# Kernel optimization log

Hardware: AMD Instinct MI355X
Metric: run time of the kernel (lower is better)

The kernel has to match this reference:

```python
import jax, jax.numpy as jnp
import numpy as np

TOKENS, IN_F, OUT_F, R = 8192, 4096, 4096, 16
NS_STEPS = 5
NS_EPS = 1e-7


def newtonschulz5(G, steps=NS_STEPS, eps=NS_EPS):
    # Quintic Newton-Schulz orthogonalization: sigma -> 1, preserving U, V.
    a, b, c = 3.4445, -4.775, 2.0315
    X = G / (jnp.linalg.norm(G) + eps)
    transposed = G.shape[0] > G.shape[1]
    if transposed:
        X = X.T
    for _ in range(steps):
        A = X @ X.T                 # [m, m]
        B = b * A + c * (A @ A)
        X = a * X + B @ X
    if transposed:
        X = X.T
    return X


def setup_inputs() -> dict:
    key = jax.random.key(0)
    kx, kw, kb, ka, kbb = jax.random.split(key, 5)
    x = jax.random.normal(kx, (TOKENS, IN_F), dtype=jnp.float32)
    # base linear params
    W = jax.random.normal(kw, (OUT_F, IN_F), dtype=jnp.float32) / np.sqrt(IN_F)
    bias = jax.random.normal(kb, (OUT_F,), dtype=jnp.float32) * 0.01
    # LoRA params: A ~ orthogonal-ish rows, B small (init_scale/sqrt(out*r))
    lora_A = jax.random.normal(ka, (R, IN_F), dtype=jnp.float32) / np.sqrt(IN_F)
    init_std = 0.01 / np.sqrt(OUT_F * R)
    lora_B = jax.random.normal(kbb, (OUT_F, R), dtype=jnp.float32) * init_std
    return {"x": x, "W": W, "bias": bias, "lora_A": lora_A, "lora_B": lora_B}


def reference(x, W, bias, lora_A, lora_B):
    # base_out = x @ W^T + bias
    base_out = x @ W.T + bias
    # G = B A  (full [out, in] materialization, as in the original)
    G = lora_B @ lora_A
    alpha = jnp.linalg.norm(G)
    M = newtonschulz5(G)
    # lora_dropout = 0 -> identity
    lora_out = x @ M.T
    return base_out + alpha * lora_out
```

## Files before the change

### kernel.cpp

```cpp
#include <hip/hip_runtime.h>
#include <hip/hip_bf16.h>
#include <math.h>

#define TOKENS 8192
#define IN_F   4096
#define OUT_F  4096
#define LR     16

typedef __bf16 bf16_t;
typedef __attribute__((ext_vector_type(8)))  __bf16 bf16x8;
typedef __attribute__((ext_vector_type(4)))  __bf16 bf16x4;
typedef __attribute__((ext_vector_type(4)))  float  floatx4;
typedef __attribute__((ext_vector_type(16))) float  floatx16;

#define GL2LDS(gp, lp) \
    __builtin_amdgcn_global_load_lds((const __attribute__((address_space(1))) unsigned int*)(gp), \
                                     (__attribute__((address_space(3))) unsigned int*)(lp), 16, 0, 0)

__global__ void pq_kernel(const float* __restrict__ A, const float* __restrict__ B,
                          float* __restrict__ P, float* __restrict__ Q) {
    __shared__ float red[256];
    const int b = blockIdx.x, t = threadIdx.x;
    float s = 0.f;
    if (b < 256) {
        const int i = b >> 4, j = b & 15;
        const float* ai = A + (size_t)i * IN_F;
        const float* aj = A + (size_t)j * IN_F;
        for (int k = t; k < IN_F; k += 256) s += ai[k] * aj[k];
    } else {
        const int i = (b - 256) >> 4, j = (b - 256) & 15;
        for (int k = t; k < OUT_F; k += 256) s += B[k * LR + i] * B[k * LR + j];
    }
    red[t] = s; __syncthreads();
    for (int off = 128; off > 0; off >>= 1) {
        if (t < off) red[t] += red[t + off];
        __syncthreads();
    }
    if (t == 0) {
        if (b < 256) P[b] = red[0];
        else         Q[b - 256] = red[0];
    }
}

__global__ void ns_kernel(const float* __restrict__ P, const float* __restrict__ Q,
                          float* __restrict__ Sc) {
    __shared__ double Ps[256], Qs[256], Ss[256], Ys[256], Zs[256], Ts[256], Us[256], Vs[256];
    __shared__ double alpha_s, inv_n;
    const int t = threadIdx.x, i = t >> 4, j = t & 15;
    Ps[t] = P[t]; Qs[t] = Q[t];
    __syncthreads();
    if (t == 0) {
        double s = 0.0;
        for (int a = 0; a < 16; ++a)
            for (int b2 = 0; b2 < 16; ++b2) s += Ps[a * 16 + b2] * Qs[b2 * 16 + a];
        const double al = sqrt(s);
        alpha_s = al;
        inv_n   = 1.0 / (al + 1e-7);
    }
    __syncthreads();
    Ss[t] = (i == j) ? inv_n : 0.0;
    __syncthreads();
    const double ca = 3.4445, cb = -4.775, cc = 2.0315;
    for (int step = 0; step < 5; ++step) {
        double s;
        s = 0; for (int q = 0; q < 16; ++q) s += Ss[i*16+q] * Ps[q*16+j]; Ys[t] = s; __syncthreads();
        s = 0; for (int q = 0; q < 16; ++q) s += Ys[i*16+q] * Ss[j*16+q]; Zs[t] = s; __syncthreads();
        s = 0; for (int q = 0; q < 16; ++q) s += Zs[i*16+q] * Qs[q*16+j]; Ts[t] = s; __syncthreads();
        s = 0; for (int q = 0; q < 16; ++q) s += Ts[i*16+q] * Ss[q*16+j]; Us[t] = s; __syncthreads();
        s = 0; for (int q = 0; q < 16; ++q) s += Ts[i*16+q] * Us[q*16+j]; Vs[t] = s; __syncthreads();
        Ss[t] = ca * Ss[t] + cb * Us[t] + cc * Vs[t];
        __syncthreads();
    }
    Sc[t] = (float)(alpha_s * Ss[t]);
}

__global__ void sca_kernel(const float* __restrict__ Sc, const float* __restrict__ A,
                           float* __restrict__ ScA) {
    const int idx = blockIdx.x * 256 + threadIdx.x;
    const int r = idx >> 12, i = idx & 4095;
    float s = 0.f;
    for (int q = 0; q < 16; ++q) s += Sc[r * 16 + q] * A[q * IN_F + i];
    ScA[r * IN_F + i] = s;
}

__global__ void prep_kernel(const float* __restrict__ x, bf16_t* __restrict__ Xb,
                            const float* __restrict__ W, const float* __restrict__ Bm,
                            const float* __restrict__ ScA, bf16_t* __restrict__ Wb) {
    const int b = blockIdx.x, t = threadIdx.x;
    if (b < 32768) {
        const int idx = b * 256 + t;
        const float4 u = ((const float4*)x)[idx];
        bf16x4 v;
        v[0] = (__bf16)u.x; v[1] = (__bf16)u.y; v[2] = (__bf16)u.z; v[3] = (__bf16)u.w;
        ((bf16x4*)Xb)[idx] = v;
        return;
    }
    const int bb = b - 32768;
    const int o0 = (bb >> 2) * 4;
    const int i  = (bb & 3) * 1024 + t * 4;
    float4 acc[4];
    #pragma unroll
    for (int r = 0; r < 4; ++r) acc[r] = *(const float4*)&W[(size_t)(o0 + r) * IN_F + i];
    #pragma unroll
    for (int q = 0; q < LR; ++q) {
        const float4 sa = *(const float4*)&ScA[q * IN_F + i];
        #pragma unroll
        for (int r = 0; r < 4; ++r) {
            const float bq = Bm[(o0 + r) * LR + q];
            acc[r].x += bq * sa.x; acc[r].y += bq * sa.y;
            acc[r].z += bq * sa.z; acc[r].w += bq * sa.w;
        }
    }
    #pragma unroll
    for (int r = 0; r < 4; ++r) {
        bf16x4 v;
        v[0] = (__bf16)acc[r].x; v[1] = (__bf16)acc[r].y;
        v[2] = (__bf16)acc[r].z; v[3] = (__bf16)acc[r].w;
        *(bf16x4*)&Wb[(size_t)(o0 + r) * IN_F + i] = v;
    }
}

#define GBM 256
#define GBN 256
#define GBK 32
#define GNT (IN_F / GBK)

__global__ __launch_bounds__(512, 2) void gemm_kernel(
        const bf16_t* __restrict__ Xb, const bf16_t* __restrict__ Wb,
        const float* __restrict__ bias, float* __restrict__ out) {
    __shared__ bf16_t lds[3 * 16384];
    const int t = threadIdx.x;
    const int lane = t & 63, wv = t >> 6;
    const int wm = wv & 1, wn = wv >> 1;
    const int ln = lane & 31, kg = lane >> 5;

    const int bid = blockIdx.x;
    const int swz = (bid & 7) * 64 + (bid >> 3);
    const int mt = swz & 31, nt = swz >> 5;
    const int m0 = mt * GBM, n0 = nt * GBN;

    const int g_lrow = t >> 3, g_sp = t & 7;
    const int g_sl = g_sp ^ (g_lrow & 7);
    const int g_r  = (g_lrow << 1) | (g_sl >> 2);
    const int g_k0 = (g_sl & 3) * 8;
    const bf16_t* srcA0 = Xb + (size_t)(m0 + g_r) * IN_F + g_k0;
    const bf16_t* srcA1 = srcA0 + (size_t)128 * IN_F;
    const bf16_t* srcB0 = Wb + (size_t)(n0 + g_r) * IN_F + g_k0;
    const bf16_t* srcB1 = srcB0 + (size_t)128 * IN_F;
    const int dA0 = t * 8, dA1 = 4096 + t * 8;

#define STAGE(buf, kt) do { \
        GL2LDS(srcA0 + (size_t)(kt) * GBK, (buf) + dA0); \
        GL2LDS(srcA1 + (size_t)(kt) * GBK, (buf) + dA1); \
        GL2LDS(srcB0 + (size_t)(kt) * GBK, (buf) + 8192 + dA0); \
        GL2LDS(srcB1 + (size_t)(kt) * GBK, (buf) + 8192 + dA1); \
    } while (0)

    const int rx  = (ln >> 1) & 7;
    const int sl0 = ((((ln & 1) << 2) | kg)       ^ rx) * 8;
    const int sl1 = ((((ln & 1) << 2) | (2 + kg)) ^ rx) * 8;
    const int aRow = (wm * 64 + (ln >> 1)) * 64;
    const int bRow = 8192 + (wn * 32 + (ln >> 1)) * 64;

    floatx16 acc[4][2];
    #pragma unroll
    for (int mf = 0; mf < 4; ++mf)
        #pragma unroll
        for (int nf = 0; nf < 2; ++nf)
            acc[mf][nf] = (floatx16)(0.0f);

    bf16_t* bc = &lds[0];
    bf16_t* bn = &lds[16384];
    bf16_t* bs = &lds[32768];

    STAGE(bc, 0);
    STAGE(bn, 1);
    asm volatile("s_waitcnt vmcnt(4)" ::: "memory");
    __builtin_amdgcn_s_barrier();
    asm volatile("" ::: "memory");

    for (int kt = 0; kt < GNT; ++kt) {
        if (kt + 2 < GNT) STAGE(bs, kt + 2);

        bf16x8 a0[4], a1[4], b0[2], b1[2];
        #pragma unroll
        for (int mf = 0; mf < 4; ++mf) {
            a0[mf] = *(const bf16x8*)&bc[aRow + mf * 1024 + sl0];
            a1[mf] = *(const bf16x8*)&bc[aRow + mf * 1024 + sl1];
        }
        #pragma unroll
        for (int nf = 0; nf < 2; ++nf) {
            b0[nf] = *(const bf16x8*)&bc[bRow + nf * 1024 + sl0];
            b1[nf] = *(const bf16x8*)&bc[bRow + nf * 1024 + sl1];
        }

        __builtin_amdgcn_s_barrier();
        asm volatile("" ::: "memory");
        __builtin_amdgcn_s_setprio(1);
        #pragma unroll
        for (int mf = 0; mf < 4; ++mf)
            #pragma unroll
            for (int nf = 0; nf < 2; ++nf)
                acc[mf][nf] = __builtin_amdgcn_mfma_f32_32x32x16_bf16(a0[mf], b0[nf], acc[mf][nf], 0, 0, 0);
        #pragma unroll
        for (int mf = 0; mf < 4; ++mf)
            #pragma unroll
            for (int nf = 0; nf < 2; ++nf)
                acc[mf][nf] = __builtin_amdgcn_mfma_f32_32x32x16_bf16(a1[mf], b1[nf], acc[mf][nf], 0, 0, 0);
        __builtin_amdgcn_s_setprio(0);

        if (kt < GNT - 2) asm volatile("s_waitcnt vmcnt(4)" ::: "memory");
        else              asm volatile("s_waitcnt vmcnt(0)" ::: "memory");
        __builtin_amdgcn_s_barrier();
        asm volatile("" ::: "memory");

        bf16_t* tmp = bc; bc = bn; bn = bs; bs = tmp;
    }
#undef STAGE

    const int colb = n0 + wn * 64 + ln;
    const int rowb = m0 + wm * 128 + 4 * kg;
    const float bv0 = bias[colb];
    const float bv1 = bias[colb + 32];
    #pragma unroll
    for (int mf = 0; mf < 4; ++mf) {
        #pragma unroll
        for (int rg = 0; rg < 16; ++rg) {
            const int row = rowb + mf * 32 + (rg & 3) + 8 * (rg >> 2);
            out[(size_t)row * OUT_F + colb]      = acc[mf][0][rg] + bv0;
            out[(size_t)row * OUT_F + colb + 32] = acc[mf][1][rg] + bv1;
        }
    }
}

extern "C" void kernel_launch(void* const* d_in, const int* in_sizes, int n_in,
                              void* d_out, int out_size, void* d_ws, size_t ws_size,
                              hipStream_t stream) {
    const float* x    = (const float*)d_in[0];
    const float* W    = (const float*)d_in[1];
    const float* bias = (const float*)d_in[2];
    const float* lA_  = (const float*)d_in[3];
    const float* lB_  = (const float*)d_in[4];
    float* out = (float*)d_out;

    char* ws = (char*)d_ws;
    bf16_t* Xb  = (bf16_t*)ws;
    bf16_t* Wb  = (bf16_t*)(ws + 67108864);
    float*  ScA = (float*)(ws + 100663296);
    float*  P   = (float*)(ws + 100925440);
    float*  Q   = P + 256;
    float*  Sc  = Q + 256;

    pq_kernel  <<<512, 256, 0, stream>>>(lA_, lB_, P, Q);
    ns_kernel  <<<1, 256, 0, stream>>>(P, Q, Sc);
    sca_kernel <<<256, 256, 0, stream>>>(Sc, lA_, ScA);
    prep_kernel<<<36864, 256, 0, stream>>>(x, Xb, W, lB_, ScA, Wb);
    gemm_kernel<<<512, 512, 0, stream>>>(Xb, Wb, bias, out);
}
```

Measured before the change: 578.4 us.

## Restructure GEMM main loop into 8-phase pipeline with 16x16x32 MFMA and BK=64

Rewrites the bf16 GEMM main loop. Each K tile of 64 is split into two 32-wide halves, and each half is split into M-half phases. LDS fragment loads, global-to-LDS staging of the next tile and MFMA bursts are interleaved, with barriers between phases. The MFMA shape moves from 32x32x16 to 16x16x32 (8x4 fragments per wave), and LDS is double-buffered over 128 KB. The intent is to overlap memory traffic with matrix math more finely and cut per-iteration overhead. The cost is many more barriers and more complex waitcnt bookkeeping, and 128 KB of LDS per block may limit occupancy to one block per CU despite launch_bounds(512,2).

```diff
diff --git a/kernel.cpp b/kernel.cpp
--- a/kernel.cpp
+++ b/kernel.cpp
@@ -120,115 +120,124 @@
     }
 }
 
-#define GBM 256
-#define GBN 256
-#define GBK 32
-#define GNT (IN_F / GBK)
+#define GNT 64
+
+#define FENCE asm volatile("" ::: "memory")
+#define BAR   do { __builtin_amdgcn_s_barrier(); FENCE; } while (0)
+
+#define STG(ubase, srcp, koff) do { \
+    GL2LDS((srcp) + (koff), &lds[(ubase) + t * 8]); \
+    GL2LDS((srcp) + (size_t)128 * IN_F + (koff), &lds[(ubase) + 4096 + t * 8]); } while (0)
+
+#define PH_A(KS, D, MH, af) do { \
+    af[0] = *(const bf16x8*)&lds[aRd + ((KS)*2+(D))*8192 + ((MH)*4+0)*512]; \
+    af[1] = *(const bf16x8*)&lds[aRd + ((KS)*2+(D))*8192 + ((MH)*4+1)*512]; \
+    af[2] = *(const bf16x8*)&lds[aRd + ((KS)*2+(D))*8192 + ((MH)*4+2)*512]; \
+    af[3] = *(const bf16x8*)&lds[aRd + ((KS)*2+(D))*8192 + ((MH)*4+3)*512]; } while (0)
+
+#define PH_B(KS, D, bfv) do { \
+    bfv[0] = *(const bf16x8*)&lds[bRd + ((KS)*2+(D))*8192 + 0*512]; \
+    bfv[1] = *(const bf16x8*)&lds[bRd + ((KS)*2+(D))*8192 + 1*512]; \
+    bfv[2] = *(const bf16x8*)&lds[bRd + ((KS)*2+(D))*8192 + 2*512]; \
+    bfv[3] = *(const bf16x8*)&lds[bRd + ((KS)*2+(D))*8192 + 3*512]; } while (0)
+
+#define MFMA16(MH, af, bfv) do { \
+    _Pragma("unroll") \
+    for (int _i = 0; _i < 4; ++_i) { \
+        acc[(MH)*4+_i][0] = __builtin_amdgcn_mfma_f32_16x16x32_bf16(af[_i], bfv[0], acc[(MH)*4+_i][0], 0, 0, 0); \
+        acc[(MH)*4+_i][1] = __builtin_amdgcn_mfma_f32_16x16x32_bf16(af[_i], bfv[1], acc[(MH)*4+_i][1], 0, 0, 0); \
+        acc[(MH)*4+_i][2] = __builtin_amdgcn_mfma_f32_16x16x32_bf16(af[_i], bfv[2], acc[(MH)*4+_i][2], 0, 0, 0); \
+        acc[(MH)*4+_i][3] = __builtin_amdgcn_mfma_f32_16x16x32_bf16(af[_i], bfv[3], acc[(MH)*4+_i][3], 0, 0, 0); \
+    } } while (0)
+
+#define KTILE(D, DN, KTN, DO_STAGE, VMN_MID, DO_VM_END) do { \
+    bf16x8 af[4]; bf16x8 bfv[4]; \
+     \
+    PH_A(0, D, 0, af); PH_B(0, D, bfv); \
+    if (DO_STAGE) STG(32768 + (DN)*8192, sB, (size_t)(KTN)*64); \
+    BAR; \
+    __builtin_amdgcn_s_setprio(1); MFMA16(0, af, bfv); __builtin_amdgcn_s_setprio(0); \
+    BAR; \
+     \
+    PH_A(0, D, 1, af); \
+    if (DO_STAGE) STG((DN)*8192, sA, (size_t)(KTN)*64); \
+    BAR; \
+    __builtin_amdgcn_s_setprio(1); MFMA16(1, af, bfv); __builtin_amdgcn_s_setprio(0); \
+    if ((VMN_MID) == 4) asm volatile("s_waitcnt vmcnt(4)" ::: "memory"); \
+    else                asm volatile("s_waitcnt vmcnt(0)" ::: "memory"); \
+    BAR; \
+     \
+    PH_A(1, D, 0, af); PH_B(1, D, bfv); \
+    if (DO_STAGE) STG(32768 + (2+(DN))*8192, sB, (size_t)(KTN)*64 + 32); \
+    BAR; \
+    __builtin_amdgcn_s_setprio(1); MFMA16(0, af, bfv); __builtin_amdgcn_s_setprio(0); \
+    BAR; \
+     \
+    PH_A(1, D, 1, af); \
+    if (DO_STAGE) STG((2+(DN))*8192, sA, (size_t)(KTN)*64 + 32); \
+    BAR; \
+    __builtin_amdgcn_s_setprio(1); MFMA16(1, af, bfv); __builtin_amdgcn_s_setprio(0); \
+    if (DO_VM_END) asm volatile("s_waitcnt vmcnt(4)" ::: "memory"); \
+    BAR; \
+} while (0)
 
 __global__ __launch_bounds__(512, 2) void gemm_kernel(
         const bf16_t* __restrict__ Xb, const bf16_t* __restrict__ Wb,
         const float* __restrict__ bias, float* __restrict__ out) {
-    __shared__ bf16_t lds[3 * 16384];
+    __shared__ bf16_t lds[65536];
     const int t = threadIdx.x;
     const int lane = t & 63, wv = t >> 6;
     const int wm = wv & 1, wn = wv >> 1;
-    const int ln = lane & 31, kg = lane >> 5;
+    const int fl = lane & 15, q = lane >> 4;
 
     const int bid = blockIdx.x;
     const int swz = (bid & 7) * 64 + (bid >> 3);
     const int mt = swz & 31, nt = swz >> 5;
-    const int m0 = mt * GBM, n0 = nt * GBN;
-
-    const int g_lrow = t >> 3, g_sp = t & 7;
-    const int g_sl = g_sp ^ (g_lrow & 7);
-    const int g_r  = (g_lrow << 1) | (g_sl >> 2);
-    const int g_k0 = (g_sl & 3) * 8;
-    const bf16_t* srcA0 = Xb + (size_t)(m0 + g_r) * IN_F + g_k0;
-    const bf16_t* srcA1 = srcA0 + (size_t)128 * IN_F;
-    const bf16_t* srcB0 = Wb + (size_t)(n0 + g_r) * IN_F + g_k0;
-    const bf16_t* srcB1 = srcB0 + (size_t)128 * IN_F;
-    const int dA0 = t * 8, dA1 = 4096 + t * 8;
-
-#define STAGE(buf, kt) do { \
-        GL2LDS(srcA0 + (size_t)(kt) * GBK, (buf) + dA0); \
-        GL2LDS(srcA1 + (size_t)(kt) * GBK, (buf) + dA1); \
-        GL2LDS(srcB0 + (size_t)(kt) * GBK, (buf) + 8192 + dA0); \
-        GL2LDS(srcB1 + (size_t)(kt) * GBK, (buf) + 8192 + dA1); \
-    } while (0)
-
-    const int rx  = (ln >> 1) & 7;
-    const int sl0 = ((((ln & 1) << 2) | kg)       ^ rx) * 8;
-    const int sl1 = ((((ln & 1) << 2) | (2 + kg)) ^ rx) * 8;
-    const int aRow = (wm * 64 + (ln >> 1)) * 64;
-    const int bRow = 8192 + (wn * 32 + (ln >> 1)) * 64;
-
-    floatx16 acc[4][2];
-    #pragma unroll
-    for (int mf = 0; mf < 4; ++mf)
+    const int m0 = mt * 256, n0 = nt * 256;
+
+    const int rx  = (fl >> 1) & 3;
+    const int aRd = (wm * 128 + fl) * 32 + ((q ^ rx) << 3);
+    const int bRd = 32768 + (wn * 64 + fl) * 32 + ((q ^ rx) << 3);
+
+    const int cS = (t & 3) ^ ((t >> 3) & 3);
+    const int rS = t >> 2;
+    const bf16_t* sA = Xb + (size_t)(m0 + rS) * IN_F + cS * 8;
+    const bf16_t* sB = Wb + (size_t)(n0 + rS) * IN_F + cS * 8;
+
+    floatx4 acc[8][4];
+    #pragma unroll
+    for (int i = 0; i < 8; ++i)
         #pragma unroll
-        for (int nf = 0; nf < 2; ++nf)
-            acc[mf][nf] = (floatx16)(0.0f);
-
-    bf16_t* bc = &lds[0];
-    bf16_t* bn = &lds[16384];
-    bf16_t* bs = &lds[32768];
-
-    STAGE(bc, 0);
-    STAGE(bn, 1);
+        for (int n = 0; n < 4; ++n) acc[i][n] = (floatx4)(0.0f);
+
+    STG(32768 + 0 * 8192, sB, 0);
+    STG(0 * 8192,         sA, 0);
+    STG(32768 + 2 * 8192, sB, 32);
+    STG(2 * 8192,         sA, 32);
     asm volatile("s_waitcnt vmcnt(4)" ::: "memory");
-    __builtin_amdgcn_s_barrier();
-    asm volatile("" ::: "memory");
-
-    for (int kt = 0; kt < GNT; ++kt) {
-        if (kt + 2 < GNT) STAGE(bs, kt + 2);
-
-        bf16x8 a0[4], a1[4], b0[2], b1[2];
+    BAR;
+
+    for (int kt2 = 0; kt2 < GNT / 2 - 1; ++kt2) {
+        const int kt = kt2 * 2;
+        KTILE(0, 1, kt + 1, true, 4, true);
+        KTILE(1, 0, kt + 2, true, 4, true);
+    }
+    KTILE(0, 1, GNT - 1, true, 4, true);
+    KTILE(1, 0, 0, false, 0, false);
+
+    const int colb = n0 + wn * 64 + fl;
+    const int rowb = m0 + wm * 128 + q * 4;
+    float bvv[4];
+    #pragma unroll
+    for (int nf = 0; nf < 4; ++nf) bvv[nf] = bias[colb + nf * 16];
+    #pragma unroll
+    for (int mf = 0; mf < 8; ++mf) {
         #pragma unroll
-        for (int mf = 0; mf < 4; ++mf) {
-            a0[mf] = *(const bf16x8*)&bc[aRow + mf * 1024 + sl0];
-            a1[mf] = *(const bf16x8*)&bc[aRow + mf * 1024 + sl1];
-        }
-        #pragma unroll
-        for (int nf = 0; nf < 2; ++nf) {
-            b0[nf] = *(const bf16x8*)&bc[bRow + nf * 1024 + sl0];
-            b1[nf] = *(const bf16x8*)&bc[bRow + nf * 1024 + sl1];
-        }
-
-        __builtin_amdgcn_s_barrier();
-        asm volatile("" ::: "memory");
-        __builtin_amdgcn_s_setprio(1);
-        #pragma unroll
-        for (int mf = 0; mf < 4; ++mf)
+        for (int rg = 0; rg < 4; ++rg) {
+            const int row = rowb + mf * 16 + rg;
             #pragma unroll
-            for (int nf = 0; nf < 2; ++nf)
-                acc[mf][nf] = __builtin_amdgcn_mfma_f32_32x32x16_bf16(a0[mf], b0[nf], acc[mf][nf], 0, 0, 0);
-        #pragma unroll
-        for (int mf = 0; mf < 4; ++mf)
-            #pragma unroll
-            for (int nf = 0; nf < 2; ++nf)
-                acc[mf][nf] = __builtin_amdgcn_mfma_f32_32x32x16_bf16(a1[mf], b1[nf], acc[mf][nf], 0, 0, 0);
-        __builtin_amdgcn_s_setprio(0);
-
-        if (kt < GNT - 2) asm volatile("s_waitcnt vmcnt(4)" ::: "memory");
-        else              asm volatile("s_waitcnt vmcnt(0)" ::: "memory");
-        __builtin_amdgcn_s_barrier();
-        asm volatile("" ::: "memory");
-
-        bf16_t* tmp = bc; bc = bn; bn = bs; bs = tmp;
-    }
-#undef STAGE
-
-    const int colb = n0 + wn * 64 + ln;
-    const int rowb = m0 + wm * 128 + 4 * kg;
-    const float bv0 = bias[colb];
-    const float bv1 = bias[colb + 32];
-    #pragma unroll
-    for (int mf = 0; mf < 4; ++mf) {
-        #pragma unroll
-        for (int rg = 0; rg < 16; ++rg) {
-            const int row = rowb + mf * 32 + (rg & 3) + 8 * (rg >> 2);
-            out[(size_t)row * OUT_F + colb]      = acc[mf][0][rg] + bv0;
-            out[(size_t)row * OUT_F + colb + 32] = acc[mf][1][rg] + bv1;
+            for (int nf = 0; nf < 4; ++nf)
+                out[(size_t)row * OUT_F + colb + nf * 16] = acc[mf][nf][rg] + bvv[nf];
         }
     }
 }
```

Result: faster. 527.2 us (-8.9%).
